# Kernel optimization log

Measured on AMD Instinct MI355X. Metric: run time of the kernel, lower is better.

## Reference

```python
import jax, jax.numpy as jnp
import numpy as np

B, R, S = 4, 16384, 96

def setup_inputs() -> dict:
    key = jax.random.key(0)
    k1, k2, k3, k4 = jax.random.split(key, 4)
    colors = jax.random.normal(k1, (B, R, S, 3), dtype=jnp.float32)
    densities = jax.random.normal(k2, (B, R, S, 1), dtype=jnp.float32)
    # depths must be monotonically increasing along the sample axis
    depths = jnp.sort(jax.random.uniform(k3, (B, R, S, 1), dtype=jnp.float32), axis=2)
    sample_coordinates = jax.random.uniform(k4, (B, R, S, 3), dtype=jnp.float32)
    return {"colors": colors, "densities": densities, "depths": depths,
            "sample_coordinates": sample_coordinates, "white_back": 0}


def reference(colors, densities, depths, sample_coordinates, white_back):
    deltas = depths[:, :, 1:] - depths[:, :, :-1]                     # [B,R,S-1,1]
    colors_mid = (colors[:, :, :-1] + colors[:, :, 1:]) * 0.5
    densities_mid = (densities[:, :, :-1] + densities[:, :, 1:]) * 0.5
    depths_mid = (depths[:, :, :-1] + depths[:, :, 1:]) * 0.5
    coords_mid = (sample_coordinates[:, :, :-1] + sample_coordinates[:, :, 1:]) * 0.5

    densities_mid = jax.nn.softplus(densities_mid)                    # activation_factory
    alpha = 1.0 - jnp.exp(-densities_mid * deltas)                    # [B,R,S-1,1]

    ones = jnp.ones_like(alpha[:, :, :1])
    alpha_shifted = jnp.concatenate([ones, 1.0 - alpha + 1e-10], axis=-2)
    trans = jnp.cumprod(alpha_shifted, axis=-2)[:, :, :-1]            # transmittance T_i

    weights = alpha * trans                                            # [B,R,S-1,1]
    tau = trans[:, :, -1, :]                                           # [B,R,1]

    composite_rgb = jnp.sum(weights * colors_mid, axis=-2)             # [B,R,3]
    composite_point = jnp.sum(weights * coords_mid, axis=-2)           # [B,R,3]
    weight_total = jnp.sum(weights, axis=2)                            # [B,R,1]

    composite_depth = jnp.sum(weights * depths_mid, axis=-2)           # [B,R,1]
    composite_depth = jnp.nan_to_num(composite_depth, nan=jnp.inf)
    composite_depth = jnp.clip(composite_depth, jnp.min(depths), jnp.max(depths))

    composite_rgb = jnp.where(white_back != 0,
                              composite_rgb + 1.0 - weight_total,
                              composite_rgb)
    return composite_rgb, composite_depth, weights, composite_point, tau
```

## Files before the change

kernel.cpp:

```cpp
#include <hip/hip_runtime.h>

#define NRAYS 65536
#define NS    96
#define NI    95

#define OFF_RGB   0
#define OFF_DEPTH 196608
#define OFF_W     262144
#define OFF_PT    6488064
#define OFF_TAU   6684672

__global__ void depth_minmax_sorted(const float* __restrict__ deps, unsigned* ws) {
    const int t = blockIdx.x * blockDim.x + threadIdx.x;
    float lo = deps[(size_t)t * NS];
    float hi = deps[(size_t)t * NS + (NS - 1)];
    #pragma unroll
    for (int off = 32; off; off >>= 1) {
        lo = fminf(lo, __shfl_xor(lo, off, 64));
        hi = fmaxf(hi, __shfl_xor(hi, off, 64));
    }
    if ((threadIdx.x & 63) == 0) {
        atomicMin(&ws[0], __float_as_uint(lo));
        atomicMin(&ws[1], ~__float_as_uint(hi));
    }
}

__device__ __forceinline__ float softplus_fast(float x) {
    return fmaxf(x, 0.0f) + __logf(1.0f + __expf(-fabsf(x)));
}

__launch_bounds__(256)
__global__ void raymarch(const float* __restrict__ colors,
                         const float* __restrict__ dens,
                         const float* __restrict__ deps,
                         const float* __restrict__ coords,
                         const int* __restrict__ wbp,
                         const unsigned* __restrict__ mm,
                         float* __restrict__ out) {
    __shared__ float s_col[16 * 288];
    __shared__ float s_crd[16 * 288];

    const int tid  = threadIdx.x;
    const int lane = tid & 63;
    const int sub  = tid & 15;
    const int r    = tid >> 4;
    const int g    = blockIdx.x * 16 + r;

    float d[6], n[6];
    {
        const float2* q = (const float2*)(deps + (size_t)g * NS) + 3 * sub;
        #pragma unroll
        for (int j = 0; j < 3; ++j) { float2 v = q[j]; d[2*j] = v.x; d[2*j+1] = v.y; }
    }
    {
        const float2* q = (const float2*)(dens + (size_t)g * NS) + 3 * sub;
        #pragma unroll
        for (int j = 0; j < 3; ++j) { float2 v = q[j]; n[2*j] = v.x; n[2*j+1] = v.y; }
    }

    {
        const float4* g1 = (const float4*)(colors + (size_t)blockIdx.x * (16 * 288));
        const float4* g2 = (const float4*)(coords + (size_t)blockIdx.x * (16 * 288));
        float4* s1 = (float4*)s_col;
        float4* s2 = (float4*)s_crd;
        #pragma unroll
        for (int k = 0; k < 4; ++k) s1[tid + 256 * k] = g1[tid + 256 * k];
        if (tid < 128) s1[tid + 1024] = g1[tid + 1024];
        #pragma unroll
        for (int k = 0; k < 4; ++k) s2[tid + 256 * k] = g2[tid + 256 * k];
        if (tid < 128) s2[tid + 1024] = g2[tid + 1024];
    }
    __syncthreads();

    float c[18], p[18];
    {
        const float2* q = (const float2*)(s_col + r * 288 + 18 * sub);
        #pragma unroll
        for (int j = 0; j < 9; ++j) { float2 v = q[j]; c[2*j] = v.x; c[2*j+1] = v.y; }
    }
    {
        const float2* q = (const float2*)(s_crd + r * 288 + 18 * sub);
        #pragma unroll
        for (int j = 0; j < 9; ++j) { float2 v = q[j]; p[2*j] = v.x; p[2*j+1] = v.y; }
    }
    const int noff = (sub < 15) ? 18 * (sub + 1) : 0;
    float cn0 = s_col[r * 288 + noff + 0];
    float cn1 = s_col[r * 288 + noff + 1];
    float cn2 = s_col[r * 288 + noff + 2];
    float pn0 = s_crd[r * 288 + noff + 0];
    float pn1 = s_crd[r * 288 + noff + 1];
    float pn2 = s_crd[r * 288 + noff + 2];
    const int nsrc = (lane & 48) | ((sub + 1) & 15);
    float d6 = __shfl(d[0], nsrc, 64);
    float n6 = __shfl(n[0], nsrc, 64);

    float a[6], f[6];
    #pragma unroll
    for (int i = 0; i < 6; ++i) {
        float dn1 = (i < 5) ? d[i+1] : d6;
        float nn1 = (i < 5) ? n[i+1] : n6;
        float E = __expf(-softplus_fast(0.5f * (n[i] + nn1)) * (dn1 - d[i]));
        const bool valid = (i < 5) || (sub < 15);
        a[i] = valid ? (1.0f - E) : 0.0f;
        f[i] = valid ? (E + 1e-10f) : 1.0f;
    }

    float incl = ((f[0] * f[1]) * (f[2] * f[3])) * (f[4] * f[5]);
    #pragma unroll
    for (int off = 1; off < 16; off <<= 1) {
        float t = __shfl_up(incl, off, 16);
        if (sub >= off) incl *= t;
    }
    float excl = __shfl_up(incl, 1, 16);
    if (sub == 0) excl = 1.0f;

    float acc[8];
    #pragma unroll
    for (int k = 0; k < 8; ++k) acc[k] = 0.0f;
    float t = excl;
    float tauc = 0.0f;
    const size_t wb = (size_t)OFF_W + (size_t)g * NI + 6 * sub;
    #pragma unroll
    for (int i = 0; i < 6; ++i) {
        float w = a[i] * t;
        if (i < 5 || sub < 15) out[wb + i] = w;
        float dn1 = (i < 5) ? d[i+1] : d6;
        float dm  = 0.5f * (d[i] + dn1);
        float cmx = 0.5f * (c[3*i+0] + ((i < 5) ? c[3*i+3] : cn0));
        float cmy = 0.5f * (c[3*i+1] + ((i < 5) ? c[3*i+4] : cn1));
        float cmz = 0.5f * (c[3*i+2] + ((i < 5) ? c[3*i+5] : cn2));
        float pmx = 0.5f * (p[3*i+0] + ((i < 5) ? p[3*i+3] : pn0));
        float pmy = 0.5f * (p[3*i+1] + ((i < 5) ? p[3*i+4] : pn1));
        float pmz = 0.5f * (p[3*i+2] + ((i < 5) ? p[3*i+5] : pn2));
        acc[0] += w * cmx;  acc[1] += w * cmy;  acc[2] += w * cmz;
        acc[3] += w * pmx;  acc[4] += w * pmy;  acc[5] += w * pmz;
        acc[6] += w * dm;   acc[7] += w;
        if (i == 4) tauc = t;
        t *= f[i];
    }
    float tau = __shfl(tauc, (lane & 48) | 15, 64);

    #pragma unroll
    for (int k = 0; k < 8; ++k) {
        #pragma unroll
        for (int off = 1; off < 16; off <<= 1)
            acc[k] += __shfl_xor(acc[k], off, 64);
    }

    if (sub == 0) {
        float add = (wbp != nullptr && wbp[0] != 0) ? (1.0f - acc[7]) : 0.0f;
        size_t rb = (size_t)OFF_RGB + (size_t)g * 3;
        out[rb + 0] = acc[0] + add;
        out[rb + 1] = acc[1] + add;
        out[rb + 2] = acc[2] + add;
        size_t pb = (size_t)OFF_PT + (size_t)g * 3;
        out[pb + 0] = acc[3];
        out[pb + 1] = acc[4];
        out[pb + 2] = acc[5];
        float cd = acc[6];
        if (cd != cd) cd = __int_as_float(0x7f800000);
        float dmin = __uint_as_float(mm[0]);
        float dmax = __uint_as_float(~mm[1]);
        cd = fminf(fmaxf(cd, dmin), dmax);
        out[OFF_DEPTH + g] = cd;
        out[OFF_TAU + g]   = tau;
    }
}

extern "C" void kernel_launch(void* const* d_in, const int* in_sizes, int n_in,
                              void* d_out, int out_size, void* d_ws, size_t ws_size,
                              hipStream_t stream) {
    const float* colors = (const float*)d_in[0];
    const float* dens   = (const float*)d_in[1];
    const float* deps   = (const float*)d_in[2];
    const float* coords = (const float*)d_in[3];
    const int*   wb     = (n_in > 4) ? (const int*)d_in[4] : nullptr;
    float* out = (float*)d_out;
    unsigned* mm = (unsigned*)d_ws;

    hipMemsetAsync(mm, 0xFF, 8, stream);
    depth_minmax_sorted<<<NRAYS / 256, 256, 0, stream>>>(deps, mm);
    raymarch<<<NRAYS / 16, 256, 0, stream>>>(colors, dens, deps, coords, wb, mm, out);
}
```

Before: 239.1 us.

## Reuse one LDS buffer for staging and coalesce weight stores via LDS

Halves the LDS footprint by loading colors and coordinates through a single shared buffer in sequence, and raises the launch-bounds occupancy hint to 8 blocks. The per-ray weights, previously written to global memory as scattered scalars, are now collected in LDS and written out as coalesced float4 stores per block. The cost is extra barriers, and the coordinate loads no longer overlap with the color loads, which can expose more latency.

```diff
diff --git a/kernel.cpp b/kernel.cpp
--- a/kernel.cpp
+++ b/kernel.cpp
@@ -29,7 +29,7 @@
     return fmaxf(x, 0.0f) + __logf(1.0f + __expf(-fabsf(x)));
 }
 
-__launch_bounds__(256)
+__launch_bounds__(256, 8)
 __global__ void raymarch(const float* __restrict__ colors,
                          const float* __restrict__ dens,
                          const float* __restrict__ deps,
@@ -37,8 +37,7 @@
                          const int* __restrict__ wbp,
                          const unsigned* __restrict__ mm,
                          float* __restrict__ out) {
-    __shared__ float s_col[16 * 288];
-    __shared__ float s_crd[16 * 288];
+    __shared__ float sbuf[16 * 288];
 
     const int tid  = threadIdx.x;
     const int lane = tid & 63;
@@ -58,38 +57,45 @@
         for (int j = 0; j < 3; ++j) { float2 v = q[j]; n[2*j] = v.x; n[2*j+1] = v.y; }
     }
 
+    float4* s4 = (float4*)sbuf;
+
     {
         const float4* g1 = (const float4*)(colors + (size_t)blockIdx.x * (16 * 288));
+        #pragma unroll
+        for (int k = 0; k < 4; ++k) s4[tid + 256 * k] = g1[tid + 256 * k];
+        if (tid < 128) s4[tid + 1024] = g1[tid + 1024];
+    }
+    __syncthreads();
+    float c[18], cn0, cn1, cn2;
+    {
+        const float2* q = (const float2*)(sbuf + r * 288 + 18 * sub);
+        #pragma unroll
+        for (int j = 0; j < 9; ++j) { float2 v = q[j]; c[2*j] = v.x; c[2*j+1] = v.y; }
+        const int noff = (sub < 15) ? 18 * (sub + 1) : 0;
+        cn0 = sbuf[r * 288 + noff + 0];
+        cn1 = sbuf[r * 288 + noff + 1];
+        cn2 = sbuf[r * 288 + noff + 2];
+    }
+    __syncthreads();
+
+    {
         const float4* g2 = (const float4*)(coords + (size_t)blockIdx.x * (16 * 288));
-        float4* s1 = (float4*)s_col;
-        float4* s2 = (float4*)s_crd;
-        #pragma unroll
-        for (int k = 0; k < 4; ++k) s1[tid + 256 * k] = g1[tid + 256 * k];
-        if (tid < 128) s1[tid + 1024] = g1[tid + 1024];
-        #pragma unroll
-        for (int k = 0; k < 4; ++k) s2[tid + 256 * k] = g2[tid + 256 * k];
-        if (tid < 128) s2[tid + 1024] = g2[tid + 1024];
-    }
-    __syncthreads();
-
-    float c[18], p[18];
-    {
-        const float2* q = (const float2*)(s_col + r * 288 + 18 * sub);
-        #pragma unroll
-        for (int j = 0; j < 9; ++j) { float2 v = q[j]; c[2*j] = v.x; c[2*j+1] = v.y; }
-    }
-    {
-        const float2* q = (const float2*)(s_crd + r * 288 + 18 * sub);
+        #pragma unroll
+        for (int k = 0; k < 4; ++k) s4[tid + 256 * k] = g2[tid + 256 * k];
+        if (tid < 128) s4[tid + 1024] = g2[tid + 1024];
+    }
+    __syncthreads();
+    float p[18], pn0, pn1, pn2;
+    {
+        const float2* q = (const float2*)(sbuf + r * 288 + 18 * sub);
         #pragma unroll
         for (int j = 0; j < 9; ++j) { float2 v = q[j]; p[2*j] = v.x; p[2*j+1] = v.y; }
-    }
-    const int noff = (sub < 15) ? 18 * (sub + 1) : 0;
-    float cn0 = s_col[r * 288 + noff + 0];
-    float cn1 = s_col[r * 288 + noff + 1];
-    float cn2 = s_col[r * 288 + noff + 2];
-    float pn0 = s_crd[r * 288 + noff + 0];
-    float pn1 = s_crd[r * 288 + noff + 1];
-    float pn2 = s_crd[r * 288 + noff + 2];
+        const int noff = (sub < 15) ? 18 * (sub + 1) : 0;
+        pn0 = sbuf[r * 288 + noff + 0];
+        pn1 = sbuf[r * 288 + noff + 1];
+        pn2 = sbuf[r * 288 + noff + 2];
+    }
+
     const int nsrc = (lane & 48) | ((sub + 1) & 15);
     float d6 = __shfl(d[0], nsrc, 64);
     float n6 = __shfl(n[0], nsrc, 64);
@@ -114,16 +120,18 @@
     float excl = __shfl_up(incl, 1, 16);
     if (sub == 0) excl = 1.0f;
 
+    __syncthreads();
+
     float acc[8];
     #pragma unroll
     for (int k = 0; k < 8; ++k) acc[k] = 0.0f;
     float t = excl;
     float tauc = 0.0f;
-    const size_t wb = (size_t)OFF_W + (size_t)g * NI + 6 * sub;
+    float* wl = sbuf + r * NI + 6 * sub;
     #pragma unroll
     for (int i = 0; i < 6; ++i) {
         float w = a[i] * t;
-        if (i < 5 || sub < 15) out[wb + i] = w;
+        if (i < 5 || sub < 15) wl[i] = w;
         float dn1 = (i < 5) ? d[i+1] : d6;
         float dm  = 0.5f * (d[i] + dn1);
         float cmx = 0.5f * (c[3*i+0] + ((i < 5) ? c[3*i+3] : cn0));
@@ -165,6 +173,14 @@
         out[OFF_DEPTH + g] = cd;
         out[OFF_TAU + g]   = tau;
     }
+
+    __syncthreads();
+    {
+        float4* o4 = (float4*)(out + OFF_W + (size_t)blockIdx.x * (16 * NI));
+        const float4* w4 = (const float4*)sbuf;
+        o4[tid] = w4[tid];
+        if (tid < 124) o4[256 + tid] = w4[256 + tid];
+    }
 }
 
 extern "C" void kernel_launch(void* const* d_in, const int* in_sizes, int n_in,
```

New measurement: 247.1 us. 1.03x slower.
